# Kernel tuning notes

Measured on AMD Instinct MI355X. Metric: run time of the kernel, lower is better.

The kernel has to match this reference:

```python
import jax, jax.numpy as jnp
import numpy as np

N = 1_000_000
DIM = 128
NUM_GRAPHS = 4096


def setup_inputs() -> dict:
    key = jax.random.key(0)
    kx, kq, kb = jax.random.split(key, 3)
    x = jax.random.normal(kx, (N, DIM), dtype=jnp.float32)
    query = jax.random.normal(kq, (DIM,), dtype=jnp.float32) * 0.02
    batch = jnp.sort(jax.random.randint(kb, (N,), 0, NUM_GRAPHS, dtype=jnp.int64))
    return {"x": x, "query": query, "batch": batch}


def reference(x, query, batch):
    # scores: [N] dot of each node feature with the learned query vector
    scores = jnp.einsum("nd,d->n", x, query)
    # segment-wise numerically-stable softmax over nodes belonging to each graph
    seg_max = jax.ops.segment_max(scores, batch, num_segments=NUM_GRAPHS)
    ex = jnp.exp(scores - seg_max[batch])  # [N]
    seg_sum = jax.ops.segment_sum(ex, batch, num_segments=NUM_GRAPHS)
    weights = ex / seg_sum[batch]  # [N]
    # weighted scatter-add pooling -> [num_graphs, dim]
    pooled = jax.ops.segment_sum(weights[:, None] * x, batch, num_segments=NUM_GRAPHS)
    return pooled
```

## Files before the change

kernel.cpp:

```cpp
#include <hip/hip_runtime.h>
#include <math.h>

#define DIM 128

__device__ __forceinline__ int lower_bound_i(const int* __restrict__ b, int n, int key) {
    int lo = 0, hi = n;
    while (lo < hi) {
        int mid = (lo + hi) >> 1;
        if (b[mid] < key) lo = mid + 1; else hi = mid;
    }
    return lo;
}

__global__ __launch_bounds__(256) void attnpool_kernel(
    const float* __restrict__ x, const float* __restrict__ q,
    const int* __restrict__ batch, float* __restrict__ out, int n)
{
    const int g    = blockIdx.x;
    const int tid  = threadIdx.x;
    const int wave = tid >> 6;
    const int lane = tid & 63;
    const int half = lane >> 5;
    const int hl   = lane & 31;

    const int lo = lower_bound_i(batch, n, g);
    const int hi = lower_bound_i(batch, n, g + 1);

    const float4 qf = *(const float4*)(q + hl * 4);

    float  m = -INFINITY;
    float  l = 0.f;
    float4 o = make_float4(0.f, 0.f, 0.f, 0.f);

    for (int i = lo + wave * 2 + half; i < hi; i += 8) {
        const float4 xv = *(const float4*)(x + (size_t)i * DIM + hl * 4);
        float s = xv.x * qf.x + xv.y * qf.y + xv.z * qf.z + xv.w * qf.w;
        s += __shfl_xor(s, 16);
        s += __shfl_xor(s, 8);
        s += __shfl_xor(s, 4);
        s += __shfl_xor(s, 2);
        s += __shfl_xor(s, 1);
        float p;
        if (s > m) {
            const float a = __expf(m - s);
            l *= a;
            o.x *= a; o.y *= a; o.z *= a; o.w *= a;
            m = s;
            p = 1.f;
        } else {
            p = __expf(s - m);
        }
        l += p;
        o.x += p * xv.x; o.y += p * xv.y; o.z += p * xv.z; o.w += p * xv.w;
    }

    __shared__ float sm_m[8];
    __shared__ float sm_l[8];
    __shared__ float sm_o[8 * DIM];
    const int idx = wave * 2 + half;
    if (hl == 0) { sm_m[idx] = m; sm_l[idx] = l; }
    *(float4*)(sm_o + idx * DIM + hl * 4) = o;
    __syncthreads();

    if (tid < DIM) {
        float M = -INFINITY;
        #pragma unroll
        for (int h = 0; h < 8; ++h)
            if (sm_l[h] > 0.f && sm_m[h] > M) M = sm_m[h];
        float L = 0.f, O = 0.f;
        #pragma unroll
        for (int h = 0; h < 8; ++h) {
            if (sm_l[h] > 0.f) {
                const float c = __expf(sm_m[h] - M);
                L += c * sm_l[h];
                O += c * sm_o[h * DIM + tid];
            }
        }
        out[(size_t)g * DIM + tid] = (L > 0.f) ? (O / L) : 0.f;
    }
}

extern "C" void kernel_launch(void* const* d_in, const int* in_sizes, int n_in,
                              void* d_out, int out_size, void* d_ws, size_t ws_size,
                              hipStream_t stream) {
    const float* x     = (const float*)d_in[0];
    const float* q     = (const float*)d_in[1];
    const int*   batch = (const int*)d_in[2];
    float*       out   = (float*)d_out;
    const int n          = in_sizes[0] / DIM;
    const int num_graphs = out_size / DIM;
    attnpool_kernel<<<num_graphs, 256, 0, stream>>>(x, q, batch, out, n);
}
```

Before: 660.3 us.

## Software-pipeline row loads in chunks of four with batched online-softmax updates

Each half-wave stream now processes four rows per iteration and prefetches the next four rows' float4 loads into registers before computing on the current ones. The shuffle reductions for the four dot products are interleaved, and the online softmax rescale happens once per chunk using the chunk maximum instead of once per row. This is meant to hide global memory latency and cut divergent branches and exp calls, at the cost of more registers and some wasted predicated loads at segment tails.

```diff
diff --git a/kernel.cpp b/kernel.cpp
--- a/kernel.cpp
+++ b/kernel.cpp
@@ -2,6 +2,10 @@
 #include <math.h>
 
 #define DIM 128
+#define CHUNK 4
+#define STREAMS 8
+#define STRIDE (STREAMS)
+#define ROUND (STREAMS * CHUNK)
 
 __device__ __forceinline__ int lower_bound_i(const int* __restrict__ b, int n, int key) {
     int lo = 0, hi = n;
@@ -22,6 +26,7 @@
     const int lane = tid & 63;
     const int half = lane >> 5;
     const int hl   = lane & 31;
+    const int sid  = wave * 2 + half;
 
     const int lo = lower_bound_i(batch, n, g);
     const int hi = lower_bound_i(batch, n, g + 1);
@@ -32,44 +37,75 @@
     float  l = 0.f;
     float4 o = make_float4(0.f, 0.f, 0.f, 0.f);
 
-    for (int i = lo + wave * 2 + half; i < hi; i += 8) {
-        const float4 xv = *(const float4*)(x + (size_t)i * DIM + hl * 4);
-        float s = xv.x * qf.x + xv.y * qf.y + xv.z * qf.z + xv.w * qf.w;
-        s += __shfl_xor(s, 16);
-        s += __shfl_xor(s, 8);
-        s += __shfl_xor(s, 4);
-        s += __shfl_xor(s, 2);
-        s += __shfl_xor(s, 1);
-        float p;
-        if (s > m) {
-            const float a = __expf(m - s);
+    const int i0 = lo + sid;
+    const float4 z = make_float4(0.f, 0.f, 0.f, 0.f);
+
+    float4 cur[CHUNK];
+    #pragma unroll
+    for (int j = 0; j < CHUNK; ++j) {
+        const int ii = i0 + j * STRIDE;
+        cur[j] = (ii < hi) ? *(const float4*)(x + (size_t)ii * DIM + hl * 4) : z;
+    }
+
+    for (int base = i0; base < hi; base += ROUND) {
+        float4 nxt[CHUNK];
+        #pragma unroll
+        for (int j = 0; j < CHUNK; ++j) {
+            const int ii = base + ROUND + j * STRIDE;
+            nxt[j] = (ii < hi) ? *(const float4*)(x + (size_t)ii * DIM + hl * 4) : z;
+        }
+
+        float s[CHUNK];
+        #pragma unroll
+        for (int j = 0; j < CHUNK; ++j)
+            s[j] = cur[j].x * qf.x + cur[j].y * qf.y + cur[j].z * qf.z + cur[j].w * qf.w;
+
+        #pragma unroll
+        for (int d = 16; d >= 1; d >>= 1) {
+            #pragma unroll
+            for (int j = 0; j < CHUNK; ++j)
+                s[j] += __shfl_xor(s[j], d);
+        }
+
+        #pragma unroll
+        for (int j = 0; j < CHUNK; ++j)
+            if (base + j * STRIDE >= hi) s[j] = -INFINITY;
+
+        const float smax = fmaxf(fmaxf(s[0], s[1]), fmaxf(s[2], s[3]));
+        if (smax > m) {
+            const float a = __expf(m - smax);
             l *= a;
             o.x *= a; o.y *= a; o.z *= a; o.w *= a;
-            m = s;
-            p = 1.f;
-        } else {
-            p = __expf(s - m);
+            m = smax;
         }
-        l += p;
-        o.x += p * xv.x; o.y += p * xv.y; o.z += p * xv.z; o.w += p * xv.w;
+
+        #pragma unroll
+        for (int j = 0; j < CHUNK; ++j) {
+            const float p = (base + j * STRIDE < hi) ? __expf(s[j] - m) : 0.f;
+            l += p;
+            o.x += p * cur[j].x; o.y += p * cur[j].y;
+            o.z += p * cur[j].z; o.w += p * cur[j].w;
+        }
+
+        #pragma unroll
+        for (int j = 0; j < CHUNK; ++j) cur[j] = nxt[j];
     }
 
-    __shared__ float sm_m[8];
-    __shared__ float sm_l[8];
-    __shared__ float sm_o[8 * DIM];
-    const int idx = wave * 2 + half;
-    if (hl == 0) { sm_m[idx] = m; sm_l[idx] = l; }
-    *(float4*)(sm_o + idx * DIM + hl * 4) = o;
+    __shared__ float sm_m[STREAMS];
+    __shared__ float sm_l[STREAMS];
+    __shared__ float sm_o[STREAMS * DIM];
+    if (hl == 0) { sm_m[sid] = m; sm_l[sid] = l; }
+    *(float4*)(sm_o + sid * DIM + hl * 4) = o;
     __syncthreads();
 
     if (tid < DIM) {
         float M = -INFINITY;
         #pragma unroll
-        for (int h = 0; h < 8; ++h)
+        for (int h = 0; h < STREAMS; ++h)
             if (sm_l[h] > 0.f && sm_m[h] > M) M = sm_m[h];
         float L = 0.f, O = 0.f;
         #pragma unroll
-        for (int h = 0; h < 8; ++h) {
+        for (int h = 0; h < STREAMS; ++h) {
             if (sm_l[h] > 0.f) {
                 const float c = __expf(sm_m[h] - M);
                 L += c * sm_l[h];
```

Result: slower. 676.1 us (+2.4%).
